# Kernel tuning notes

Measured on AMD Instinct MI355X. Metric: run time of the kernel, lower is better.

The kernel has to match this reference:

```python
import jax, jax.numpy as jnp
import numpy as np

N_BONES = 8
NV = 14062
PARENTS = [-1, 0, 1, 2, 3, 4, 5, 6]  # kinematic chain


def rotvec_to_rotmat(rv):
    # rv: [..., 3] -> [..., 3, 3] via Rodrigues
    ang = jnp.sqrt(jnp.sum(rv * rv, axis=-1) + 1e-12)  # [...]
    k = rv / ang[..., None]
    kx, ky, kz = k[..., 0], k[..., 1], k[..., 2]
    z = jnp.zeros_like(kx)
    K = jnp.stack([
        jnp.stack([z, -kz, ky], -1),
        jnp.stack([kz, z, -kx], -1),
        jnp.stack([-ky, kx, z], -1)], -2)  # [...,3,3]
    s = jnp.sin(ang)[..., None, None]
    c = jnp.cos(ang)[..., None, None]
    I = jnp.eye(3, dtype=rv.dtype)
    return I + s * K + (1.0 - c) * (K @ K)


def bilinear_sample(img, gx, gy):
    # img: [H, W]; gx, gy: [B, Nv] normalized coords in [-1,1]
    # bilinear, border padding, align_corners=True (matches F.grid_sample)
    H, W = img.shape
    x = jnp.clip((gx + 1.0) * 0.5 * (W - 1), 0.0, W - 1.0)
    y = jnp.clip((gy + 1.0) * 0.5 * (H - 1), 0.0, H - 1.0)
    x0 = jnp.floor(x); y0 = jnp.floor(y)
    x0i = x0.astype(jnp.int32); y0i = y0.astype(jnp.int32)
    x1i = jnp.minimum(x0i + 1, W - 1); y1i = jnp.minimum(y0i + 1, H - 1)
    wx = x - x0; wy = y - y0
    v00 = img[y0i, x0i]; v01 = img[y0i, x1i]
    v10 = img[y1i, x0i]; v11 = img[y1i, x1i]
    return (v00 * (1 - wx) + v01 * wx) * (1 - wy) + (v10 * (1 - wx) + v11 * wx) * wy


def setup_inputs() -> dict:
    key = jax.random.key(0)
    ks = jax.random.split(key, 12)
    B = 256
    theta = jax.random.normal(ks[0], (B, N_BONES, 3), jnp.float32) * 0.3
    tau = jax.random.normal(ks[1], (B, 1), jnp.float32) * 0.1
    alpha = jax.random.uniform(ks[2], (B, 1), jnp.float32)
    bsw = jax.random.uniform(ks[3], (B, 55), jnp.float32)
    W = jax.random.uniform(ks[4], (N_BONES, NV), jnp.float32) + 1e-3
    W = W / W.sum(axis=0, keepdims=True)  # done in HACK.__init__
    T = jax.random.normal(ks[5], (NV, 3), jnp.float32)
    P = jax.random.normal(ks[6], (N_BONES, 3, 3, NV, 3), jnp.float32) * 0.01
    L = jax.random.uniform(ks[7], (1, 1, 256, 256), jnp.float32)
    ts = jax.random.normal(ks[8], (NV, 3), jnp.float32)
    # L2P: per-bone rigid transforms (rotation + small translation)
    rv = jax.random.normal(ks[9], (N_BONES, 3), jnp.float32) * 0.2
    R = rotvec_to_rotmat(rv)
    t = jax.random.normal(ks[10], (N_BONES, 3), jnp.float32) * 0.1
    L2P = jnp.tile(jnp.eye(4, dtype=jnp.float32), (N_BONES, 1, 1))
    L2P = L2P.at[:, :3, :3].set(R).at[:, :3, 3].set(t)
    E = jax.random.normal(ks[11], (55, NV, 3), jnp.float32) * 0.05
    uvgrid = jax.random.uniform(jax.random.fold_in(key, 99), (NV, 2), jnp.float32)
    return {"theta": theta, "tau": tau, "alpha": alpha, "bsw": bsw, "W": W,
            "T": T, "P": P, "L": L, "ts": ts, "L2P": L2P, "E": E, "uvgrid": uvgrid}


def reference(theta, tau, alpha, bsw, W, T, P, L, ts, L2P, E, uvgrid):
    B = theta.shape[0]
    R = rotvec_to_rotmat(theta)  # [B, Nb, 3, 3]
    # theta_matrix_zero: bone 0 subtracts itself (-> 0), others subtract I
    sub = jnp.concatenate([R[:, :1],
                           jnp.broadcast_to(jnp.eye(3, dtype=R.dtype), (B, N_BONES - 1, 3, 3))], axis=1)
    theta_zero = R - sub  # [B, Nb, 3, 3]
    # pose-corrective blendshapes: sum over (bone, i, j)
    P_theta = jnp.einsum('bnij,nijvk->bvk', theta_zero, P)  # [B, Nv, 3]

    # forward kinematics along chain: L2W_pose[i] = L2W_pose[parent] @ (L2P[i] @ local[i])
    local = jnp.tile(jnp.eye(4, dtype=R.dtype), (B, N_BONES, 1, 1))
    local = local.at[:, :, :3, :3].set(R)  # [B, Nb, 4, 4]
    mats = []
    for i in range(N_BONES):
        Ai = jnp.einsum('ij,bjk->bik', L2P[i], local[:, i])
        if PARENTS[i] >= 0:
            Ai = jnp.matmul(mats[PARENTS[i]], Ai)
        mats.append(Ai)
    L2W_pose = jnp.stack(mats, axis=1)  # [B, Nb, 4, 4]

    # rest-pose world-to-local (inverse bind matrices)
    rest = []
    for i in range(N_BONES):
        rest.append(L2P[i] if PARENTS[i] < 0 else rest[PARENTS[i]] @ L2P[i])
    W2L = jnp.linalg.inv(jnp.stack(rest))  # [Nb, 4, 4]

    W2L2pWs = jnp.einsum('bnij,njk->bnik', L2W_pose, W2L)  # [B, Nb, 4, 4]
    # skinning-weight contraction over bones -> per-vertex 4x4 transform
    M = jnp.einsum('bnij,nv->bvij', W2L2pWs, W)  # [B, Nv, 4, 4]

    # larynx displacement via grid_sample
    uv = uvgrid * 2.0 - 1.0  # [Nv, 2]
    gx = jnp.broadcast_to(uv[None, :, 0], (B, uv.shape[0]))
    gy = uv[None, :, 1] + tau * 2.0  # shift y by tau*2 (F.pad(tau*2,[1,0]))
    dist = bilinear_sample(L[0, 0], gx, gy)  # [B, Nv]
    L_tau = dist[:, :, None] * ts[None]  # [B, Nv, 3]

    T_theta = (T[None] + P_theta
               + jnp.einsum('bn,nvk->bvk', bsw, E)
               + L_tau * alpha[:, :, None])  # [B, Nv, 3]

    # homogeneous per-vertex 4x4 matvec, keep xyz
    T_transformed = (jnp.einsum('bvij,bvj->bvi', M[:, :, :3, :3], T_theta)
                     + M[:, :, :3, 3])
    return T_transformed
```

## Files before the change

kernel.cpp:

```cpp
#include <hip/hip_runtime.h>
#include <cmath>

#define NB     8
#define NVERT  14062
#define NV3    42186
#define BATCH  256
#define BBLK   32
#define NBT    8
#define KP     63
#define KE     55
#define KTOT   118
#define KPAD   120
#define KALLOC 128
#define VT     64

__device__ inline void mat4mul(const float* A, const float* B, float* C) {
#pragma unroll
  for (int i = 0; i < 4; i++)
#pragma unroll
    for (int j = 0; j < 4; j++) {
      float s = 0.f;
#pragma unroll
      for (int k = 0; k < 4; k++) s = fmaf(A[i*4+k], B[k*4+j], s);
      C[i*4+j] = s;
    }
}

__global__ void setup_kernel(const float* __restrict__ theta,
                             const float* __restrict__ bsw,
                             const float* __restrict__ L2P,
                             float* __restrict__ coef_t,
                             float* __restrict__ mats)
{
  int b = blockIdx.x * blockDim.x + threadIdx.x;
  if (b >= BATCH) return;

  float R[NB][9];
#pragma unroll
  for (int n = 0; n < NB; n++) {
    float rx = theta[(b*NB+n)*3+0];
    float ry = theta[(b*NB+n)*3+1];
    float rz = theta[(b*NB+n)*3+2];
    float ang = sqrtf(rx*rx + ry*ry + rz*rz + 1e-12f);
    float kx = rx/ang, ky = ry/ang, kz = rz/ang;
    float s = sinf(ang), c = cosf(ang);
    float K[9] = {0.f,-kz,ky,  kz,0.f,-kx,  -ky,kx,0.f};
    float K2[9];
#pragma unroll
    for (int i = 0; i < 3; i++)
#pragma unroll
      for (int j = 0; j < 3; j++) {
        float v = 0.f;
#pragma unroll
        for (int k = 0; k < 3; k++) v = fmaf(K[i*3+k], K[k*3+j], v);
        K2[i*3+j] = v;
      }
#pragma unroll
    for (int e = 0; e < 9; e++) {
      int i = e/3, j = e%3;
      R[n][e] = (i==j ? 1.f : 0.f) + s*K[e] + (1.f-c)*K2[e];
    }
  }

#pragma unroll
  for (int n = 1; n < NB; n++)
#pragma unroll
    for (int e = 0; e < 9; e++) {
      int i = e/3, j = e%3;
      coef_t[((n-1)*9+e)*BATCH + b] = R[n][e] - (i==j ? 1.f : 0.f);
    }
  for (int s2 = 0; s2 < KE; s2++)
    coef_t[(KP+s2)*BATCH + b] = bsw[b*KE + s2];
  for (int r = KTOT; r < KALLOC; r++)
    coef_t[(size_t)r*BATCH + b] = 0.f;

  float prevPose[16], prevRest[16];
#pragma unroll 1
  for (int n = 0; n < NB; n++) {
    float loc[16] = {R[n][0],R[n][1],R[n][2],0.f,
                     R[n][3],R[n][4],R[n][5],0.f,
                     R[n][6],R[n][7],R[n][8],0.f,
                     0.f,0.f,0.f,1.f};
    float A[16], pose[16], rest[16];
    mat4mul(&L2P[n*16], loc, A);
    if (n == 0) {
#pragma unroll
      for (int q = 0; q < 16; q++) { pose[q] = A[q]; rest[q] = L2P[q]; }
    } else {
      mat4mul(prevPose, A, pose);
      mat4mul(prevRest, &L2P[n*16], rest);
    }
    float w2l[16];
#pragma unroll
    for (int i = 0; i < 3; i++) {
#pragma unroll
      for (int j = 0; j < 3; j++) w2l[i*4+j] = rest[j*4+i];
      w2l[i*4+3] = -(rest[0*4+i]*rest[0*4+3] + rest[1*4+i]*rest[1*4+3] + rest[2*4+i]*rest[2*4+3]);
    }
    w2l[12]=0.f; w2l[13]=0.f; w2l[14]=0.f; w2l[15]=1.f;
    float skin[16];
    mat4mul(pose, w2l, skin);
#pragma unroll
    for (int i = 0; i < 3; i++)
#pragma unroll
      for (int j = 0; j < 4; j++)
        mats[(size_t)b*96 + n*12 + i*4 + j] = skin[i*4+j];
#pragma unroll
    for (int q = 0; q < 16; q++) { prevPose[q] = pose[q]; prevRest[q] = rest[q]; }
  }
}

__global__ __launch_bounds__(256) void fused_kernel(
    const float* __restrict__ P, const float* __restrict__ E,
    const float* __restrict__ coef_t, const float* __restrict__ matsg,
    const float* __restrict__ Wm, const float* __restrict__ T,
    const float* __restrict__ ts, const float* __restrict__ uvgrid,
    const float* __restrict__ Limg, const float* __restrict__ tau,
    const float* __restrict__ alpha, float* __restrict__ out)
{
  int bid = blockIdx.x;
  int x  = (bid >> 3) & 7;
  int y  = ((bid >> 6) << 3) | (bid & 7);
  if (y >= (NVERT + VT - 1) / VT) return;

  __shared__ float mlds[BBLK][96];
  __shared__ float ta_s[BBLK], al_s[BBLK];

  int tid  = threadIdx.x;
  int lane = tid & 63;
  int wv   = tid >> 6;
  int bbase = x * BBLK;
  int vbase = y * VT;
  int v = vbase + lane;
  bool vok = v < NVERT;
  int vc = vok ? v : NVERT - 1;
  int voffi = vc * 3;

#pragma unroll
  for (int r = 0; r < 3; r++) {
    int q = tid + r*256;
    int bb = q / 24, chunk = q - bb*24;
    *reinterpret_cast<float4*>(&mlds[bb][chunk*4]) =
        *reinterpret_cast<const float4*>(matsg + (size_t)(bbase+bb)*96 + chunk*4);
  }
  if (tid < BBLK) { ta_s[tid] = tau[bbase+tid]; al_s[tid] = alpha[bbase+tid]; }
  __syncthreads();

  const float* Pb = P + (size_t)9 * NV3;
  const float* cbase = coef_t + bbase + wv*NBT;

  float acc[NBT][3];
#pragma unroll
  for (int j = 0; j < NBT; j++) { acc[j][0]=0.f; acc[j][1]=0.f; acc[j][2]=0.f; }

  float dA0,dA1,dA2, dB0,dB1,dB2, dC0,dC1,dC2;
  float4 cA0,cA1, cB0,cB1, cC0,cC1;

#define LOAD_ROW(cn, D0,D1,D2, C0,C1)                                    \
  {                                                                      \
    int cd = (cn) <= (KTOT-1) ? (cn) : (KTOT-1);                         \
    const float* rp = (cd < KP) ? (Pb + (size_t)cd*NV3)                  \
                                : (E + (size_t)(cd-KP)*NV3);             \
    D0 = rp[voffi+0]; D1 = rp[voffi+1]; D2 = rp[voffi+2];                \
    const float* cp = cbase + (size_t)(cn)*BATCH;                        \
    C0 = *reinterpret_cast<const float4*>(cp+0);                         \
    C1 = *reinterpret_cast<const float4*>(cp+4);                         \
  }

#define FMA_ROW(D0,D1,D2, C0,C1)                                         \
  {                                                                      \
    float cf[NBT] = {C0.x,C0.y,C0.z,C0.w, C1.x,C1.y,C1.z,C1.w};          \
    _Pragma("unroll")                                                    \
    for (int j = 0; j < NBT; j++) {                                      \
      acc[j][0] = fmaf(cf[j], D0, acc[j][0]);                            \
      acc[j][1] = fmaf(cf[j], D1, acc[j][1]);                            \
      acc[j][2] = fmaf(cf[j], D2, acc[j][2]);                            \
    }                                                                    \
  }

  LOAD_ROW(0, dA0,dA1,dA2, cA0,cA1);
  LOAD_ROW(1, dB0,dB1,dB2, cB0,cB1);
  LOAD_ROW(2, dC0,dC1,dC2, cC0,cC1);

#pragma unroll 1
  for (int c = 0; c < KPAD; c += 3) {
    FMA_ROW(dA0,dA1,dA2, cA0,cA1);  LOAD_ROW(c+3, dA0,dA1,dA2, cA0,cA1);
    FMA_ROW(dB0,dB1,dB2, cB0,cB1);  LOAD_ROW(c+4, dB0,dB1,dB2, cB0,cB1);
    FMA_ROW(dC0,dC1,dC2, cC0,cC1);  LOAD_ROW(c+5, dC0,dC1,dC2, cC0,cC1);
  }

  float W8[NB];
#pragma unroll
  for (int n = 0; n < NB; n++) W8[n] = Wm[(size_t)n*NVERT + vc];
  float T0 = T[vc*3+0], T1 = T[vc*3+1], T2 = T[vc*3+2];
  float s0 = ts[vc*3+0], s1 = ts[vc*3+1], s2 = ts[vc*3+2];
  float u0 = uvgrid[vc*2+0], u1 = uvgrid[vc*2+1];

  float xc = fminf(fmaxf(u0*255.f, 0.f), 255.f);
  float xf = floorf(xc);
  int x0i = (int)xf;
  int x1i = min(x0i+1, 255);
  float wx = xc - xf;

#pragma unroll
  for (int j = 0; j < NBT; j++) {
    int bl = wv*NBT + j;
    float yc = fminf(fmaxf((u1 + ta_s[bl])*255.f, 0.f), 255.f);
    float yf = floorf(yc);
    int y0i = (int)yf;
    int y1i = min(y0i+1, 255);
    float wy = yc - yf;
    float v00 = Limg[y0i*256 + x0i], v01 = Limg[y0i*256 + x1i];
    float v10 = Limg[y1i*256 + x0i], v11 = Limg[y1i*256 + x1i];
    float dist = (v00*(1.f-wx) + v01*wx)*(1.f-wy) + (v10*(1.f-wx) + v11*wx)*wy;
    float da = dist * al_s[bl];

    float xv0 = acc[j][0] + T0 + da*s0;
    float xv1 = acc[j][1] + T1 + da*s1;
    float xv2 = acc[j][2] + T2 + da*s2;

    float o[3];
#pragma unroll
    for (int i = 0; i < 3; i++) {
      float c0=0.f, c1=0.f, c2=0.f, c3=0.f;
#pragma unroll
      for (int n = 0; n < NB; n++) {
        float4 m = *reinterpret_cast<const float4*>(&mlds[bl][n*12 + i*4]);
        float w = W8[n];
        c0 = fmaf(w, m.x, c0); c1 = fmaf(w, m.y, c1);
        c2 = fmaf(w, m.z, c2); c3 = fmaf(w, m.w, c3);
      }
      o[i] = fmaf(c0, xv0, fmaf(c1, xv1, fmaf(c2, xv2, c3)));
    }
    if (vok) {
      size_t off = (size_t)(bbase + bl)*NV3 + (size_t)v*3;
      out[off+0] = o[0];
      out[off+1] = o[1];
      out[off+2] = o[2];
    }
  }
}

extern "C" void kernel_launch(void* const* d_in, const int* in_sizes, int n_in,
                              void* d_out, int out_size, void* d_ws, size_t ws_size,
                              hipStream_t stream)
{
  const float* theta  = (const float*)d_in[0];
  const float* tau    = (const float*)d_in[1];
  const float* alpha  = (const float*)d_in[2];
  const float* bsw    = (const float*)d_in[3];
  const float* Wm     = (const float*)d_in[4];
  const float* T      = (const float*)d_in[5];
  const float* P      = (const float*)d_in[6];
  const float* L      = (const float*)d_in[7];
  const float* ts     = (const float*)d_in[8];
  const float* L2P    = (const float*)d_in[9];
  const float* E      = (const float*)d_in[10];
  const float* uvgrid = (const float*)d_in[11];
  float* out = (float*)d_out;

  float* coef_t = (float*)d_ws;
  float* mats   = coef_t + (size_t)KALLOC * BATCH;

  setup_kernel<<<dim3(4), dim3(64), 0, stream>>>(theta, bsw, L2P, coef_t, mats);
  fused_kernel<<<dim3(1792), dim3(256), 0, stream>>>(
      P, E, coef_t, mats, Wm, T, ts, uvgrid, L, tau, alpha, out);
}
```

Measured before the change: 216.2 us.

## Retile fused kernel: 256 vertices x 16 batches per block, coefs staged in LDS

```diff
diff --git a/kernel.cpp b/kernel.cpp
--- a/kernel.cpp
+++ b/kernel.cpp
@@ -5,14 +5,15 @@
 #define NVERT  14062
 #define NV3    42186
 #define BATCH  256
-#define BBLK   32
-#define NBT    8
+#define BBLK   16
+#define NBT    16
 #define KP     63
 #define KE     55
 #define KTOT   118
 #define KPAD   120
 #define KALLOC 128
-#define VT     64
+#define VBLK   256
+#define NVB    56
 
 __device__ inline void mat4mul(const float* A, const float* B, float* C) {
 #pragma unroll
@@ -110,7 +111,7 @@
   }
 }
 
-__global__ __launch_bounds__(256) void fused_kernel(
+__global__ __launch_bounds__(256, 4) void fused_kernel(
     const float* __restrict__ P, const float* __restrict__ E,
     const float* __restrict__ coef_t, const float* __restrict__ matsg,
     const float* __restrict__ Wm, const float* __restrict__ T,
@@ -119,57 +120,74 @@
     const float* __restrict__ alpha, float* __restrict__ out)
 {
   int bid = blockIdx.x;
-  int x  = (bid >> 3) & 7;
-  int y  = ((bid >> 6) << 3) | (bid & 7);
-  if (y >= (NVERT + VT - 1) / VT) return;
-
-  __shared__ float mlds[BBLK][96];
-  __shared__ float ta_s[BBLK], al_s[BBLK];
+  int r  = bid & 7;
+  int t  = bid >> 3;
+  int x  = t & 15;
+  int y  = ((t >> 4) << 3) | r;
+  if (y * VBLK >= NVERT) return;
+
+  __shared__ float clds[KALLOC][NBT];
+  __shared__ float mlds[NBT][96];
+  __shared__ float ta_s[NBT], al_s[NBT];
 
   int tid  = threadIdx.x;
   int lane = tid & 63;
   int wv   = tid >> 6;
   int bbase = x * BBLK;
-  int vbase = y * VT;
-  int v = vbase + lane;
+  int vbase = y * VBLK;
+  int v = vbase + wv*64 + lane;
   bool vok = v < NVERT;
   int vc = vok ? v : NVERT - 1;
   int voffi = vc * 3;
 
 #pragma unroll
-  for (int r = 0; r < 3; r++) {
-    int q = tid + r*256;
+  for (int rep = 0; rep < 2; rep++) {
+    int q = tid + rep*256;
+    int row = q >> 2, i4 = q & 3;
+    *reinterpret_cast<float4*>(&clds[row][i4*4]) =
+        *reinterpret_cast<const float4*>(coef_t + (size_t)row*BATCH + bbase + i4*4);
+  }
+  {
+    int q = tid;
     int bb = q / 24, chunk = q - bb*24;
     *reinterpret_cast<float4*>(&mlds[bb][chunk*4]) =
         *reinterpret_cast<const float4*>(matsg + (size_t)(bbase+bb)*96 + chunk*4);
-  }
-  if (tid < BBLK) { ta_s[tid] = tau[bbase+tid]; al_s[tid] = alpha[bbase+tid]; }
+    q = tid + 256;
+    if (q < 384) {
+      bb = q / 24; chunk = q - bb*24;
+      *reinterpret_cast<float4*>(&mlds[bb][chunk*4]) =
+          *reinterpret_cast<const float4*>(matsg + (size_t)(bbase+bb)*96 + chunk*4);
+    }
+  }
+  if (tid < NBT) { ta_s[tid] = tau[bbase+tid]; al_s[tid] = alpha[bbase+tid]; }
   __syncthreads();
 
   const float* Pb = P + (size_t)9 * NV3;
-  const float* cbase = coef_t + bbase + wv*NBT;
 
   float acc[NBT][3];
 #pragma unroll
   for (int j = 0; j < NBT; j++) { acc[j][0]=0.f; acc[j][1]=0.f; acc[j][2]=0.f; }
 
   float dA0,dA1,dA2, dB0,dB1,dB2, dC0,dC1,dC2;
-  float4 cA0,cA1, cB0,cB1, cC0,cC1;
-
-#define LOAD_ROW(cn, D0,D1,D2, C0,C1)                                    \
+  float4 cA0,cA1,cA2,cA3, cB0,cB1,cB2,cB3, cC0,cC1,cC2,cC3;
+
+#define LOAD_ROW(cn, D0,D1,D2, C0,C1,C2,C3)                              \
   {                                                                      \
     int cd = (cn) <= (KTOT-1) ? (cn) : (KTOT-1);                         \
     const float* rp = (cd < KP) ? (Pb + (size_t)cd*NV3)                  \
                                 : (E + (size_t)(cd-KP)*NV3);             \
     D0 = rp[voffi+0]; D1 = rp[voffi+1]; D2 = rp[voffi+2];                \
-    const float* cp = cbase + (size_t)(cn)*BATCH;                        \
+    const float* cp = &clds[(cn)][0];                                    \
     C0 = *reinterpret_cast<const float4*>(cp+0);                         \
     C1 = *reinterpret_cast<const float4*>(cp+4);                         \
-  }
-
-#define FMA_ROW(D0,D1,D2, C0,C1)                                         \
+    C2 = *reinterpret_cast<const float4*>(cp+8);                         \
+    C3 = *reinterpret_cast<const float4*>(cp+12);                        \
+  }
+
+#define FMA_ROW(D0,D1,D2, C0,C1,C2,C3)                                   \
   {                                                                      \
-    float cf[NBT] = {C0.x,C0.y,C0.z,C0.w, C1.x,C1.y,C1.z,C1.w};          \
+    float cf[NBT] = {C0.x,C0.y,C0.z,C0.w, C1.x,C1.y,C1.z,C1.w,           \
+                     C2.x,C2.y,C2.z,C2.w, C3.x,C3.y,C3.z,C3.w};          \
     _Pragma("unroll")                                                    \
     for (int j = 0; j < NBT; j++) {                                      \
       acc[j][0] = fmaf(cf[j], D0, acc[j][0]);                            \
@@ -178,15 +196,18 @@
     }                                                                    \
   }
 
-  LOAD_ROW(0, dA0,dA1,dA2, cA0,cA1);
-  LOAD_ROW(1, dB0,dB1,dB2, cB0,cB1);
-  LOAD_ROW(2, dC0,dC1,dC2, cC0,cC1);
+  LOAD_ROW(0, dA0,dA1,dA2, cA0,cA1,cA2,cA3);
+  LOAD_ROW(1, dB0,dB1,dB2, cB0,cB1,cB2,cB3);
+  LOAD_ROW(2, dC0,dC1,dC2, cC0,cC1,cC2,cC3);
 
 #pragma unroll 1
   for (int c = 0; c < KPAD; c += 3) {
-    FMA_ROW(dA0,dA1,dA2, cA0,cA1);  LOAD_ROW(c+3, dA0,dA1,dA2, cA0,cA1);
-    FMA_ROW(dB0,dB1,dB2, cB0,cB1);  LOAD_ROW(c+4, dB0,dB1,dB2, cB0,cB1);
-    FMA_ROW(dC0,dC1,dC2, cC0,cC1);  LOAD_ROW(c+5, dC0,dC1,dC2, cC0,cC1);
+    FMA_ROW(dA0,dA1,dA2, cA0,cA1,cA2,cA3);
+    LOAD_ROW(c+3, dA0,dA1,dA2, cA0,cA1,cA2,cA3);
+    FMA_ROW(dB0,dB1,dB2, cB0,cB1,cB2,cB3);
+    LOAD_ROW(c+4, dB0,dB1,dB2, cB0,cB1,cB2,cB3);
+    FMA_ROW(dC0,dC1,dC2, cC0,cC1,cC2,cC3);
+    LOAD_ROW(c+5, dC0,dC1,dC2, cC0,cC1,cC2,cC3);
   }
 
   float W8[NB];
@@ -204,8 +225,7 @@
 
 #pragma unroll
   for (int j = 0; j < NBT; j++) {
-    int bl = wv*NBT + j;
-    float yc = fminf(fmaxf((u1 + ta_s[bl])*255.f, 0.f), 255.f);
+    float yc = fminf(fmaxf((u1 + ta_s[j])*255.f, 0.f), 255.f);
     float yf = floorf(yc);
     int y0i = (int)yf;
     int y1i = min(y0i+1, 255);
@@ -213,7 +233,7 @@
     float v00 = Limg[y0i*256 + x0i], v01 = Limg[y0i*256 + x1i];
     float v10 = Limg[y1i*256 + x0i], v11 = Limg[y1i*256 + x1i];
     float dist = (v00*(1.f-wx) + v01*wx)*(1.f-wy) + (v10*(1.f-wx) + v11*wx)*wy;
-    float da = dist * al_s[bl];
+    float da = dist * al_s[j];
 
     float xv0 = acc[j][0] + T0 + da*s0;
     float xv1 = acc[j][1] + T1 + da*s1;
@@ -225,7 +245,7 @@
       float c0=0.f, c1=0.f, c2=0.f, c3=0.f;
 #pragma unroll
       for (int n = 0; n < NB; n++) {
-        float4 m = *reinterpret_cast<const float4*>(&mlds[bl][n*12 + i*4]);
+        float4 m = *reinterpret_cast<const float4*>(&mlds[j][n*12 + i*4]);
         float w = W8[n];
         c0 = fmaf(w, m.x, c0); c1 = fmaf(w, m.y, c1);
         c2 = fmaf(w, m.z, c2); c3 = fmaf(w, m.w, c3);
@@ -233,7 +253,7 @@
       o[i] = fmaf(c0, xv0, fmaf(c1, xv1, fmaf(c2, xv2, c3)));
     }
     if (vok) {
-      size_t off = (size_t)(bbase + bl)*NV3 + (size_t)v*3;
+      size_t off = (size_t)(bbase + j)*NV3 + (size_t)v*3;
       out[off+0] = o[0];
       out[off+1] = o[1];
       out[off+2] = o[2];
@@ -263,6 +283,6 @@
   float* mats   = coef_t + (size_t)KALLOC * BATCH;
 
   setup_kernel<<<dim3(4), dim3(64), 0, stream>>>(theta, bsw, L2P, coef_t, mats);
-  fused_kernel<<<dim3(1792), dim3(256), 0, stream>>>(
+  fused_kernel<<<dim3(896), dim3(256), 0, stream>>>(
       P, E, coef_t, mats, Wm, T, ts, uvgrid, L, tau, alpha, out);
 }
```

Measured after the change: 646.5 us. 199% more time.
